# Optimization experiments

Hardware: AMD Instinct MI355X
Metric: run time of the kernel (lower is better)

Reference implementation:

```python
import jax, jax.numpy as jnp
import numpy as np

HEADS, DH = 8, 32

def _ln(x):
    m = x.mean(-1, keepdims=True)
    v = ((x - m) ** 2).mean(-1, keepdims=True)
    return (x - m) * jax.lax.rsqrt(v + 1e-5)

def _attn(xq, xk, ei, ea, wq, wk, wv, we, wo):
    # one relation: q from dst-type nodes xq, k/v from src-type nodes xk
    Nd, Ns, E = xq.shape[0], xk.shape[0], ea.shape[0]
    src, dst = ei[0], ei[1]
    q = (xq @ wq).reshape(Nd, HEADS, DH)
    k = (xk @ wk).reshape(Ns, HEADS, DH)
    v = (xk @ wv).reshape(Ns, HEADS, DH)
    e = (ea @ we).reshape(E, HEADS, DH)
    s = jnp.sum(q[dst] * (k[src] + e), axis=-1) * (DH ** -0.5)  # (E, heads)
    m = jax.ops.segment_max(s, dst, num_segments=Nd)
    m = jnp.where(jnp.isfinite(m), m, 0.0)
    ex = jnp.exp(s - m[dst])
    den = jax.ops.segment_sum(ex, dst, num_segments=Nd)
    msg = jax.ops.segment_sum(ex[:, :, None] * (v[src] + e), dst, num_segments=Nd)
    msg = msg / (den[:, :, None] + 1e-9)
    return msg.reshape(Nd, HEADS * DH) @ wo

def setup_inputs() -> dict:
    key = jax.random.key(0)
    ks = list(jax.random.split(key, 24))
    N, H, ED, L, F = 18432, 256, 64, 2, 512
    EA, ES = 294912, 65536
    nrm = lambda k, shp, s=1.0: jax.random.normal(k, shp, dtype=jnp.float32) * s
    inp = {}
    inp['all_feats_left'] = nrm(ks[0], (N, H))
    inp['all_feats_right'] = nrm(ks[1], (N, H))
    inp['ea_ll'] = nrm(ks[2], (EA, ED))
    inp['ea_rr'] = nrm(ks[3], (EA, ED))
    inp['ea_lr'] = nrm(ks[4], (ES, ED))
    inp['ea_rl'] = nrm(ks[5], (ES, ED))
    inp['ei_ll'] = jax.random.randint(ks[6], (2, EA), 0, N, dtype=jnp.int32)
    inp['ei_rr'] = jax.random.randint(ks[7], (2, EA), 0, N, dtype=jnp.int32)
    inp['ei_lr'] = jax.random.randint(ks[8], (2, ES), 0, N, dtype=jnp.int32)
    inp['ei_rl'] = jax.random.randint(ks[9], (2, ES), 0, N, dtype=jnp.int32)
    # relation order: 0=ll, 1=rr, 2=lr (src left -> dst right), 3=rl
    inp['Wq'] = nrm(ks[10], (L, 4, H, H), H ** -0.5)
    inp['Wk'] = nrm(ks[11], (L, 4, H, H), H ** -0.5)
    inp['Wv'] = nrm(ks[12], (L, 4, H, H), H ** -0.5)
    inp['We'] = nrm(ks[13], (L, 4, ED, H), ED ** -0.5)
    inp['Wo'] = nrm(ks[14], (L, 4, H, H), H ** -0.5)
    inp['ffn_w1'] = nrm(ks[15], (L, 2, H, F), H ** -0.5)
    inp['ffn_b1'] = jnp.zeros((L, 2, F), jnp.float32)
    inp['ffn_w2'] = nrm(ks[16], (L, 2, F, H), F ** -0.5)
    inp['ffn_b2'] = jnp.zeros((L, 2, H), jnp.float32)
    inp['head_w1'] = nrm(ks[17], (H, H), H ** -0.5)
    inp['head_b1'] = jnp.zeros((H,), jnp.float32)
    inp['head_w2'] = nrm(ks[18], (H, 7), H ** -0.5)
    inp['head_b2'] = jnp.zeros((7,), jnp.float32)
    inp['action_start'] = 2048  # slice(K, None), K current nodes per arm
    return inp

def reference(all_feats_left, all_feats_right, ea_ll, ea_rr, ea_lr, ea_rl,
              Wq, Wk, Wv, We, Wo, ffn_w1, ffn_b1, ffn_w2, ffn_b2,
              head_w1, head_b1, head_w2, head_b2,
              ei_ll, ei_rr, ei_lr, ei_rl, action_start):
    xl, xr = all_feats_left, all_feats_right
    L = Wq.shape[0]
    for l in range(L):
        agg_l = (_attn(xl, xl, ei_ll, ea_ll, Wq[l, 0], Wk[l, 0], Wv[l, 0], We[l, 0], Wo[l, 0])
                 + _attn(xl, xr, ei_rl, ea_rl, Wq[l, 3], Wk[l, 3], Wv[l, 3], We[l, 3], Wo[l, 3]))
        agg_r = (_attn(xr, xr, ei_rr, ea_rr, Wq[l, 1], Wk[l, 1], Wv[l, 1], We[l, 1], Wo[l, 1])
                 + _attn(xr, xl, ei_lr, ea_lr, Wq[l, 2], Wk[l, 2], Wv[l, 2], We[l, 2], Wo[l, 2]))
        xl = _ln(xl + agg_l)
        xr = _ln(xr + agg_r)
        xl = _ln(xl + jax.nn.gelu(xl @ ffn_w1[l, 0] + ffn_b1[l, 0]) @ ffn_w2[l, 0] + ffn_b2[l, 0])
        xr = _ln(xr + jax.nn.gelu(xr @ ffn_w1[l, 1] + ffn_b1[l, 1]) @ ffn_w2[l, 1] + ffn_b2[l, 1])
    la = xl[action_start:]
    ra = xr[action_start:]
    head = lambda z: jax.nn.gelu(z @ head_w1 + head_b1) @ head_w2 + head_b2
    return head(la), head(ra)
```

## Files before the change

kernel.cpp:

```cpp
#include <hip/hip_runtime.h>
#include <math.h>

typedef __attribute__((ext_vector_type(8))) short short8;
typedef __attribute__((ext_vector_type(4))) float f32x4;

__device__ __forceinline__ unsigned short f2bf(float f) {
  unsigned u = __builtin_bit_cast(unsigned, f);
  u += 0x7fff + ((u >> 16) & 1);
  return (unsigned short)(u >> 16);
}
__device__ __forceinline__ float bf2f(unsigned short h) {
  unsigned u = ((unsigned)h) << 16;
  return __builtin_bit_cast(float, u);
}
__device__ __forceinline__ float gelu_f(float x) {
  const float c0 = 0.7978845608028654f;
  return 0.5f * x * (1.0f + tanhf(c0 * (x + 0.044715f * x * x * x)));
}
__device__ __forceinline__ void gload16(const unsigned short* g, unsigned short* l) {
  __builtin_amdgcn_global_load_lds(
      (const __attribute__((address_space(1))) unsigned int*)g,
      (__attribute__((address_space(3))) unsigned int*)l, 16, 0, 0);
}

template<bool BIAS, bool GELU>
__global__ __launch_bounds__(256)
void gemm_mfma2_k(const unsigned short* __restrict__ A0, const unsigned short* __restrict__ A1,
                  int lda,
                  const unsigned short* __restrict__ BT0, const unsigned short* __restrict__ BT1,
                  const float* __restrict__ bias0, const float* __restrict__ bias1,
                  float* __restrict__ Cf0, float* __restrict__ Cf1, int Sf, int ldf,
                  unsigned short* __restrict__ Cb10, unsigned short* __restrict__ Cb11,
                  int S2, int ldb1,
                  unsigned short* __restrict__ Cb20, unsigned short* __restrict__ Cb21, int ldb2,
                  int M, int N, int K)
{
  const int z = blockIdx.z;
  const unsigned short* A  = z ? A1  : A0;
  const unsigned short* BT = z ? BT1 : BT0;
  const float* bias        = z ? bias1 : bias0;
  float* Cf                = z ? Cf1 : Cf0;
  unsigned short* Cb1      = z ? Cb11 : Cb10;
  unsigned short* Cb2      = z ? Cb21 : Cb20;

  __shared__ __align__(16) unsigned short As[128 * 32];
  __shared__ __align__(16) unsigned short Bs[128 * 32];
  const int tid = threadIdx.x;
  const int bm = blockIdx.x * 128, bn = blockIdx.y * 128;
  const int lane = tid & 63, w = tid >> 6;
  const int wr = w >> 1, wc = w & 1;
  const int l15 = lane & 15, kg = lane >> 4;

  const int srow0 = w * 16 + (lane >> 2);
  const int srow1 = 64 + srow0;
  const int sslot = lane & 3;
  const int koff0 = (((sslot - (srow0 >> 1)) & 3)) * 8;
  const int koff1 = (((sslot - (srow1 >> 1)) & 3)) * 8;
  const unsigned short* gA0 = A + (size_t)(bm + srow0) * lda + koff0;
  const unsigned short* gA1 = A + (size_t)(bm + srow1) * lda + koff1;
  const unsigned short* gB0 = BT + (size_t)(bn + srow0) * K + koff0;
  const unsigned short* gB1 = BT + (size_t)(bn + srow1) * K + koff1;
  unsigned short* lA0 = As + w * 512;
  unsigned short* lA1 = As + 2048 + w * 512;
  unsigned short* lB0 = Bs + w * 512;
  unsigned short* lB1 = Bs + 2048 + w * 512;

  int roffA[4], roffB[4];
#pragma unroll
  for (int m = 0; m < 4; ++m) {
    int row = wr * 64 + m * 16 + l15;
    roffA[m] = row * 32 + ((kg + (row >> 1)) & 3) * 8;
  }
#pragma unroll
  for (int n = 0; n < 4; ++n) {
    int col = wc * 64 + n * 16 + l15;
    roffB[n] = col * 32 + ((kg + (col >> 1)) & 3) * 8;
  }

  f32x4 acc[4][4] = {};

  for (int k0 = 0; k0 < K; k0 += 32) {
    gload16(gA0 + k0, lA0);
    gload16(gA1 + k0, lA1);
    gload16(gB0 + k0, lB0);
    gload16(gB1 + k0, lB1);
    __syncthreads();
    short8 af[4], bfr[4];
#pragma unroll
    for (int m = 0; m < 4; ++m) af[m] = *(const short8*)(As + roffA[m]);
#pragma unroll
    for (int n = 0; n < 4; ++n) bfr[n] = *(const short8*)(Bs + roffB[n]);
#pragma unroll
    for (int m = 0; m < 4; ++m)
#pragma unroll
      for (int n = 0; n < 4; ++n)
        acc[m][n] = __builtin_amdgcn_mfma_f32_16x16x32_bf16(af[m], bfr[n], acc[m][n], 0, 0, 0);
    __syncthreads();
  }

#pragma unroll
  for (int m = 0; m < 4; ++m) {
#pragma unroll
    for (int n = 0; n < 4; ++n) {
      int col = bn + wc * 64 + n * 16 + l15;
      float bv = BIAS ? bias[col] : 0.f;
      f32x4 v = acc[m][n];
#pragma unroll
      for (int r2 = 0; r2 < 4; ++r2) {
        int row = bm + wr * 64 + m * 16 + kg * 4 + r2;
        float val = v[r2] + bv;
        if (GELU) val = gelu_f(val);
        if (col < Sf) {
          Cf[(size_t)row * ldf + col] = val;
        } else if (col < S2) {
          Cb1[(size_t)row * ldb1 + (col - Sf)] = f2bf(val);
        } else {
          Cb2[(size_t)row * ldb2 + (col - S2)] = f2bf(val);
        }
      }
    }
  }
}

__global__ __launch_bounds__(256)
void gemm_mfma4_k(const unsigned short* __restrict__ Ax0, const unsigned short* __restrict__ Ax1,
                  const unsigned short* __restrict__ Ax2, const unsigned short* __restrict__ Ax3,
                  const unsigned short* __restrict__ Bx0, const unsigned short* __restrict__ Bx1,
                  const unsigned short* __restrict__ Bx2, const unsigned short* __restrict__ Bx3,
                  unsigned short* __restrict__ Cx0, unsigned short* __restrict__ Cx1,
                  unsigned short* __restrict__ Cx2, unsigned short* __restrict__ Cx3,
                  int ldb01, int ldb23, int N01, int N23, int lda, int K, int M)
{
  const int z = blockIdx.z;
  const unsigned short* A; const unsigned short* BT; unsigned short* C;
  int ldb, Nz;
  if (z == 0)      { A = Ax0; BT = Bx0; C = Cx0; ldb = ldb01; Nz = N01; }
  else if (z == 1) { A = Ax1; BT = Bx1; C = Cx1; ldb = ldb01; Nz = N01; }
  else if (z == 2) { A = Ax2; BT = Bx2; C = Cx2; ldb = ldb23; Nz = N23; }
  else             { A = Ax3; BT = Bx3; C = Cx3; ldb = ldb23; Nz = N23; }
  const int bm = blockIdx.x * 128, bn = blockIdx.y * 128;
  if (bn >= Nz) return;

  __shared__ __align__(16) unsigned short As[128 * 32];
  __shared__ __align__(16) unsigned short Bs[128 * 32];
  const int tid = threadIdx.x;
  const int lane = tid & 63, w = tid >> 6;
  const int wr = w >> 1, wc = w & 1;
  const int l15 = lane & 15, kg = lane >> 4;
  const int srow0 = w * 16 + (lane >> 2);
  const int srow1 = 64 + srow0;
  const int sslot = lane & 3;
  const int koff0 = (((sslot - (srow0 >> 1)) & 3)) * 8;
  const int koff1 = (((sslot - (srow1 >> 1)) & 3)) * 8;
  const unsigned short* gA0 = A + (size_t)(bm + srow0) * lda + koff0;
  const unsigned short* gA1 = A + (size_t)(bm + srow1) * lda + koff1;
  const unsigned short* gB0 = BT + (size_t)(bn + srow0) * K + koff0;
  const unsigned short* gB1 = BT + (size_t)(bn + srow1) * K + koff1;
  unsigned short* lA0 = As + w * 512;
  unsigned short* lA1 = As + 2048 + w * 512;
  unsigned short* lB0 = Bs + w * 512;
// ... 27 lines not shown
    for (int m = 0; m < 4; ++m)
#pragma unroll
      for (int n = 0; n < 4; ++n)
        acc[m][n] = __builtin_amdgcn_mfma_f32_16x16x32_bf16(af[m], bfr[n], acc[m][n], 0, 0, 0);
    __syncthreads();
  }
#pragma unroll
  for (int m = 0; m < 4; ++m) {
#pragma unroll
    for (int n = 0; n < 4; ++n) {
      int col = bn + wc * 64 + n * 16 + l15;
      f32x4 v = acc[m][n];
#pragma unroll
      for (int r2 = 0; r2 < 4; ++r2) {
        int row = bm + wr * 64 + m * 16 + kg * 4 + r2;
        C[(size_t)row * ldb + col] = f2bf(v[r2]);
      }
    }
  }
}

template<bool BIAS>
__global__ __launch_bounds__(256)
void gemm_k2(const float* __restrict__ A0, const float* __restrict__ A1,
             const float* __restrict__ B, const float* __restrict__ bias,
             float* __restrict__ C0, float* __restrict__ C1,
             int M, int N, int K)
{
  const float* A = blockIdx.z ? A1 : A0;
  float* C = blockIdx.z ? C1 : C0;
  __shared__ float As[16][132];
// ... 66 lines not shown
    }
  }
}

__global__ void tc_k(const float* __restrict__ in, unsigned short* __restrict__ out,
                     int K, int N, int inStride, int outStride, int rowOff, int totK, int kOff)
{
  const int mat = blockIdx.y;
  const int idx = blockIdx.x * 256 + threadIdx.x;
  if (idx >= N * K) return;
  const int n = idx / K, k = idx - n * K;
  out[(size_t)mat * outStride + (size_t)(rowOff + n) * totK + kOff + k] =
      f2bf(in[(size_t)mat * inStride + (size_t)k * N + n]);
}

__global__ void tc_qkv_k(const float* __restrict__ Wq, const float* __restrict__ Wk,
                         const float* __restrict__ Wv, unsigned short* __restrict__ out)
{
  const int zz = blockIdx.z;
  const float* in = (zz == 0) ? Wq : (zz == 1) ? Wk : Wv;
  const int rowOff = (zz == 0) ? 0 : (zz == 1) ? 768 : 1024;
  const int mat = blockIdx.y;
  const int idx = blockIdx.x * 256 + threadIdx.x;
  const int n = idx >> 8, k = idx & 255;
  out[(size_t)mat * 327680 + (size_t)(rowOff + n) * 256 + k] =
      f2bf(in[(size_t)mat * 65536 + (size_t)k * 256 + n]);
}

__global__ __launch_bounds__(256)
void wqe_k(unsigned short* __restrict__ BT, const float* __restrict__ We, int matStride)
{
  const int mat = blockIdx.y;
  const int oc = blockIdx.x;
  const int g = oc >> 6, cc = oc & 63;
  const int kin = threadIdx.x;
  const float* wrow = We + (size_t)mat * 16384 + (size_t)cc * 256 + g * 32;
  const unsigned short* bq = BT + (size_t)mat * matStride + (size_t)(g * 32) * 256 + kin;
  float acc = 0.f;
#pragma unroll 8
  for (int d = 0; d < 32; ++d)
    acc += bf2f(bq[(size_t)d * 256]) * wrow[d];
  BT[(size_t)mat * matStride + (size_t)(256 + oc) * 256 + kin] = f2bf(acc);
}

__global__ void wo_tc_k(const float* __restrict__ Wo, unsigned short* __restrict__ BTwoF)
{
  const int mat = blockIdx.y;
  const int idx = blockIdx.x * 256 + threadIdx.x;
  const int n = idx >> 8, k = idx & 255;
  const int l = mat >> 2, i = mat & 3;
  const int side = (i == 1 || i == 2) ? 1 : 0;
  const int base = (i >= 2) ? 768 : 0;
  BTwoF[(size_t)(l * 2 + side) * 393216 + (size_t)n * 1536 + base + k] =
      f2bf(Wo[(size_t)mat * 65536 + (size_t)k * 256 + n]);
}

__global__ __launch_bounds__(256)
// ... 4 lines not shown
  const int j = blockIdx.x;
  const int h = j >> 6, c = j & 63;
  const int n = threadIdx.x;
  const float* wep = We + (size_t)mat * 16384 + (size_t)c * 256 + h * 32;
  const float* wop = Wo + (size_t)mat * 65536 + (size_t)(h * 32) * 256 + n;
  float acc = 0.f;
#pragma unroll 8
  for (int d = 0; d < 32; ++d)
    acc += wep[d] * wop[(size_t)d * 256];
  const int l = mat >> 2, i = mat & 3;
  const int side = (i == 1 || i == 2) ? 1 : 0;
  const int base = (i >= 2) ? 768 : 0;
  BTwoF[(size_t)(l * 2 + side) * 393216 + (size_t)n * 1536 + base + 256 + j] = f2bf(acc);
}

template<bool EABF>
__global__ __launch_bounds__(256)
void edge2_k(const int* __restrict__ o0, const int* __restrict__ o1,
             const int2* __restrict__ p0, const int2* __restrict__ p1,
             const void* __restrict__ e0, const void* __restrict__ e1,
             unsigned short* q0, unsigned short* q1,
             const unsigned short* __restrict__ k0, const unsigned short* __restrict__ k1,
             int Nn)
{
  const int y = blockIdx.y;
  const int* offs = y ? o1 : o0;
  const int2* pairs = y ? p1 : p0;
  const void* eaP = y ? e1 : e0;
  unsigned short* qTmsg = y ? q1 : q0;
  const unsigned short* kv = y ? k1 : k0;
  const int wv = (blockIdx.x * blockDim.x + threadIdx.x) >> 6;
  if (wv >= Nn) return;
  const int lane = threadIdx.x & 63;
  const int g = lane >> 3, p = lane & 7;
  const float scale = 0.17677669529663687f;
  const ushort4 qu = *(const ushort4*)(qTmsg + (size_t)wv * 1536 + lane * 4);
  const float qx = bf2f(qu.x), qy = bf2f(qu.y), qz = bf2f(qu.z), qw = bf2f(qu.w);
  const unsigned short* Tp = qTmsg + (size_t)wv * 1536 + 256 + g * 64 + p * 8;
  const ushort4 tu0 = *(const ushort4*)Tp;
  const ushort4 tu1 = *(const ushort4*)(Tp + 4);
  const float Ta0 = bf2f(tu0.x), Ta1 = bf2f(tu0.y), Ta2 = bf2f(tu0.z), Ta3 = bf2f(tu0.w);
  const float Tc0 = bf2f(tu1.x), Tc1 = bf2f(tu1.y), Tc2 = bf2f(tu1.z), Tc3 = bf2f(tu1.w);
  float m = -INFINITY, den = 0.f;
  float ax = 0.f, ay = 0.f, az = 0.f, aw = 0.f;
  float G[8] = {0,0,0,0,0,0,0,0};
  const int e0i = __builtin_amdgcn_readfirstlane(offs[wv]);
  const int e1i = __builtin_amdgcn_readfirstlane(offs[wv + 1]);
  for (int j = e0i; j < e1i; j += 2) {
    const bool hasB = (j + 1) < e1i;
    const int2 prA = pairs[j];
    const int2 prB = hasB ? pairs[j + 1] : prA;
    float eA[8], eB[8];
    if (EABF) {
      const unsigned short* ebp = (const unsigned short*)eaP;
      const short8 eAu = *(const short8*)(ebp + (size_t)prA.x * 64 + p * 8);
      const short8 eBu = *(const short8*)(ebp + (size_t)prB.x * 64 + p * 8);
#pragma unroll
      for (int i = 0; i < 8; ++i) {
        eA[i] = bf2f((unsigned short)eAu[i]);
        eB[i] = bf2f((unsigned short)eBu[i]);
      }
    } else {
      const float* efp = (const float*)eaP;
      const float4 a0 = *(const float4*)(efp + (size_t)prA.x * 64 + p * 8);
      const float4 a1 = *(const float4*)(efp + (size_t)prA.x * 64 + p * 8 + 4);
      const float4 b0 = *(const float4*)(efp + (size_t)prB.x * 64 + p * 8);
      const float4 b1 = *(const float4*)(efp + (size_t)prB.x * 64 + p * 8 + 4);
      eA[0]=a0.x; eA[1]=a0.y; eA[2]=a0.z; eA[3]=a0.w;
      eA[4]=a1.x; eA[5]=a1.y; eA[6]=a1.z; eA[7]=a1.w;
      eB[0]=b0.x; eB[1]=b0.y; eB[2]=b0.z; eB[3]=b0.w;
      eB[4]=b1.x; eB[5]=b1.y; eB[6]=b1.z; eB[7]=b1.w;
    }
    const unsigned short* kpA = kv + (size_t)prA.y * 512 + lane * 4;
    const unsigned short* kpB = kv + (size_t)prB.y * 512 + lane * 4;
    const ushort4 kAu = *(const ushort4*)kpA;
    const ushort4 vAu = *(const ushort4*)(kpA + 256);
    const ushort4 kBu = *(const ushort4*)kpB;
    const ushort4 vBu = *(const ushort4*)(kpB + 256);
    float pA = qx * bf2f(kAu.x) + qy * bf2f(kAu.y) + qz * bf2f(kAu.z) + qw * bf2f(kAu.w);
    pA += eA[0]*Ta0 + eA[1]*Ta1 + eA[2]*Ta2 + eA[3]*Ta3;
    pA += eA[4]*Tc0 + eA[5]*Tc1 + eA[6]*Tc2 + eA[7]*Tc3;
    float pB = qx * bf2f(kBu.x) + qy * bf2f(kBu.y) + qz * bf2f(kBu.z) + qw * bf2f(kBu.w);
    pB += eB[0]*Ta0 + eB[1]*Ta1 + eB[2]*Ta2 + eB[3]*Ta3;
    pB += eB[4]*Tc0 + eB[5]*Tc1 + eB[6]*Tc2 + eB[7]*Tc3;
    pA += __shfl_xor(pA, 1, 64); pA += __shfl_xor(pA, 2, 64); pA += __shfl_xor(pA, 4, 64);
    pB += __shfl_xor(pB, 1, 64); pB += __shfl_xor(pB, 2, 64); pB += __shfl_xor(pB, 4, 64);
    const float sA = pA * scale;
    const float sB = hasB ? pB * scale : -INFINITY;
    const float mn = fmaxf(m, fmaxf(sA, sB));
    const float corr = __expf(m - mn);
    const float wA = __expf(sA - mn);
    const float wB = __expf(sB - mn);
    m = mn;
    den = den * corr + wA + wB;
    ax = ax * corr + wA * bf2f(vAu.x) + wB * bf2f(vBu.x);
    ay = ay * corr + wA * bf2f(vAu.y) + wB * bf2f(vBu.y);
    az = az * corr + wA * bf2f(vAu.z) + wB * bf2f(vBu.z);
    aw = aw * corr + wA * bf2f(vAu.w) + wB * bf2f(vBu.w);
#pragma unroll
    for (int i = 0; i < 8; ++i)
      G[i] = G[i] * corr + wA * eA[i] + wB * eB[i];
  }
  const float inv = 1.f / (den + 1e-9f);
  ushort4 o;
  o.x = f2bf(ax * inv); o.y = f2bf(ay * inv);
  o.z = f2bf(az * inv); o.w = f2bf(aw * inv);
  *(ushort4*)(qTmsg + (size_t)wv * 1536 + lane * 4) = o;
  short8 gn;
#pragma unroll
  for (int i = 0; i < 8; ++i) gn[i] = (short)f2bf(G[i] * inv);
  *(short8*)(qTmsg + (size_t)wv * 1536 + 256 + g * 64 + p * 8) = gn;
}

__global__ __launch_bounds__(256)
void add_ln2_k(unsigned short* __restrict__ xbL, const unsigned short* __restrict__ addL,
               unsigned short* __restrict__ xbR, const unsigned short* __restrict__ addR, int Nn)
// ... 23 lines not shown
  ob.z = f2bf(d.z * r); ob.w = f2bf(d.w * r);
  *(ushort4*)(xb + (size_t)wv * 256 + lane * 4) = ob;
}

__global__ void cvt_x2_k(const float* __restrict__ aL, unsigned short* __restrict__ xbL,
                         const float* __restrict__ aR, unsigned short* __restrict__ xbR, int n4)
{
  const float* a = blockIdx.y ? aR : aL;
  unsigned short* xb = blockIdx.y ? xbR : xbL;
  int i = blockIdx.x * 256 + threadIdx.x;
  if (i >= n4) return;
  float4 v = ((const float4*)a)[i];
  ushort4 b;
  b.x = f2bf(v.x); b.y = f2bf(v.y); b.z = f2bf(v.z); b.w = f2bf(v.w);
  ((ushort4*)xb)[i] = b;
}

__global__ void cvt_ea1_k(const float* __restrict__ src, unsigned short* __restrict__ dst, int n8)
{
  int i = blockIdx.x * 256 + threadIdx.x;
  if (i >= n8) return;
  float4 a = ((const float4*)src)[i * 2];
  float4 b = ((const float4*)src)[i * 2 + 1];
  short8 o;
  o[0] = (short)f2bf(a.x); o[1] = (short)f2bf(a.y);
  o[2] = (short)f2bf(a.z); o[3] = (short)f2bf(a.w);
  o[4] = (short)f2bf(b.x); o[5] = (short)f2bf(b.y);
  o[6] = (short)f2bf(b.z); o[7] = (short)f2bf(b.w);
  *(short8*)(dst + (size_t)i * 8) = o;
}

__global__ void zero4_k(int* p, int n) {
  int i = blockIdx.x * 256 + threadIdx.x;
  if (i < n) p[i] = 0;
}
__global__ void hist4_k(const int* d0, const int* d1, const int* d2, const int* d3,
                        int E0, int E1, int E2, int E3, int* cnt, int Nn) {
  const int s = blockIdx.y;
  const int* d = (s == 0) ? d0 : (s == 1) ? d1 : (s == 2) ? d2 : d3;
  const int E = (s == 0) ? E0 : (s == 1) ? E1 : (s == 2) ? E2 : E3;
  int e = blockIdx.x * 256 + threadIdx.x;
  if (e < E) atomicAdd(&cnt[s * Nn + d[e]], 1);
}
__global__ __launch_bounds__(256)
// ... 72 lines not shown
  const int astart = Nn - Mh;
  float* out = (float*)d_out;

  char* wsp = (char*)d_ws;
  auto alloc = [&](size_t bytes) -> void* {
    void* pp = (void*)wsp;
    wsp += (bytes + 255) & ~(size_t)255;
    return pp;
  };
  unsigned short* xlb = (unsigned short*)alloc((size_t)Nn * 256 * 2);
  unsigned short* xrb = (unsigned short*)alloc((size_t)Nn * 256 * 2);
  unsigned short* aggLb = (unsigned short*)alloc((size_t)Nn * 256 * 2);
  unsigned short* aggRb = (unsigned short*)alloc((size_t)Nn * 256 * 2);
  unsigned short* qTmsgA = (unsigned short*)alloc((size_t)Nn * 1536 * 2);
  unsigned short* qTmsgB = (unsigned short*)alloc((size_t)Nn * 1536 * 2);
  unsigned short* kvbA = (unsigned short*)alloc((size_t)Nn * 512 * 2);
  unsigned short* kvbB = (unsigned short*)alloc((size_t)Nn * 512 * 2);
  unsigned short* BTqkvT = (unsigned short*)alloc((size_t)8 * 1280 * 256 * 2);
  unsigned short* BTwoF  = (unsigned short*)alloc((size_t)4 * 256 * 1536 * 2);
  unsigned short* BTf1   = (unsigned short*)alloc((size_t)4 * 512 * 256 * 2);
  unsigned short* BTf2   = (unsigned short*)alloc((size_t)4 * 256 * 512 * 2);
  unsigned short* BTh1   = (unsigned short*)alloc((size_t)256 * 256 * 2);
  unsigned short* eabf0  = (unsigned short*)alloc((size_t)E[0] * 64 * 2);
  int* offs4 = (int*)alloc((size_t)4 * (Nn + 1) * 4);
  int* cnt4  = (int*)alloc((size_t)4 * Nn * 4);
  int* cur4  = (int*)alloc((size_t)4 * Nn * 4);
  int2* pairs[4];
  for (int s = 0; s < 4; ++s) pairs[s] = (int2*)alloc((size_t)E[s] * 8);

  const dim3 B256(256);
  const int wgNodes = (Nn * 64 + 255) / 256;
  int maxE = E[0];
  for (int s = 1; s < 4; ++s) if (E[s] > maxE) maxE = E[s];

  cvt_x2_k<<<dim3((Nn * 64 + 255) / 256, 2), B256, 0, stream>>>(afl, xlb, afr, xrb, Nn * 64);
  cvt_ea1_k<<<dim3((E[0] * 8 + 255) / 256), B256, 0, stream>>>(eaA[0], eabf0, E[0] * 8);
  zero4_k<<<dim3((4 * Nn + 255) / 256), B256, 0, stream>>>(cnt4, 4 * Nn);
  {
    dim3 gh((maxE + 255) / 256, 4);
    hist4_k<<<gh, B256, 0, stream>>>(eiA[0] + E[0], eiA[1] + E[1], eiA[2] + E[2], eiA[3] + E[3],
                                     E[0], E[1], E[2], E[3], cnt4, Nn);
    scan4_k<<<dim3(4), B256, 0, stream>>>(cnt4, offs4, cur4, Nn);
    scatter4_k<<<gh, B256, 0, stream>>>(eiA[0], eiA[1], eiA[2], eiA[3],
                                        E[0], E[1], E[2], E[3], cur4,
                                        pairs[0], pairs[1], pairs[2], pairs[3], Nn);
  }
  {
    tc_qkv_k<<<dim3(256, 8, 3), B256, 0, stream>>>(Wq, Wk, Wv, BTqkvT);
    wqe_k<<<dim3(512, 8), B256, 0, stream>>>(BTqkvT, We, 327680);
    wo_tc_k<<<dim3(256, 8), B256, 0, stream>>>(Wo, BTwoF);
    wc_k<<<dim3(512, 8), B256, 0, stream>>>(We, Wo, BTwoF);
    tc_k<<<dim3((131072 + 255) / 256, 4), B256, 0, stream>>>(fw1, BTf1, 256, 512, 131072, 131072, 0, 256, 0);
    tc_k<<<dim3((131072 + 255) / 256, 4), B256, 0, stream>>>(fw2, BTf2, 512, 256, 131072, 131072, 0, 512, 0);
    tc_k<<<dim3((65536 + 255) / 256, 1), B256, 0, stream>>>(hw1, BTh1, 256, 256, 0, 0, 0, 256, 0);
  }

  auto mfma2 = [&](const unsigned short* A0, const unsigned short* A1, int lda,
                   const unsigned short* BT0, const unsigned short* BT1,
                   const float* bias0, const float* bias1,
                   float* Cf0, float* Cf1, int Sf, int ldf,
                   unsigned short* Cb10, unsigned short* Cb11, int S2, int ldb1,
                   unsigned short* Cb20, unsigned short* Cb21, int ldb2,
                   int M, int N, int K, bool biasf, bool gelu) {
    dim3 g(M / 128, N / 128, 2);
    if (biasf && gelu)
      gemm_mfma2_k<true, true ><<<g, B256, 0, stream>>>(A0, A1, lda, BT0, BT1, bias0, bias1,
          Cf0, Cf1, Sf, ldf, Cb10, Cb11, S2, ldb1, Cb20, Cb21, ldb2, M, N, K);
    else if (biasf)
      gemm_mfma2_k<true, false><<<g, B256, 0, stream>>>(A0, A1, lda, BT0, BT1, bias0, bias1,
          Cf0, Cf1, Sf, ldf, Cb10, Cb11, S2, ldb1, Cb20, Cb21, ldb2, M, N, K);
    else
      gemm_mfma2_k<false, false><<<g, B256, 0, stream>>>(A0, A1, lda, BT0, BT1, bias0, bias1,
          Cf0, Cf1, Sf, ldf, Cb10, Cb11, S2, ldb1, Cb20, Cb21, ldb2, M, N, K);
  };

  for (int l = 0; l < 2; ++l) {
    const unsigned short* btLL = BTqkvT + (size_t)(l*4+0) * 327680;
    const unsigned short* btRR = BTqkvT + (size_t)(l*4+1) * 327680;
    const unsigned short* btLR = BTqkvT + (size_t)(l*4+2) * 327680;
    const unsigned short* btRL = BTqkvT + (size_t)(l*4+3) * 327680;
    mfma2(xlb, xrb, 256, btLL, btRR, nullptr, nullptr, nullptr, nullptr, 0, 0,
          qTmsgA, qTmsgB, 768, 1536, kvbA, kvbB, 512, Nn, 1280, 256, false, false);
    edge2_k<true><<<dim3(wgNodes, 1), B256, 0, stream>>>(
        offs4, offs4, pairs[0], pairs[0], eabf0, eabf0, qTmsgA, qTmsgA, kvbA, kvbA, Nn);
    edge2_k<false><<<dim3(wgNodes, 1), B256, 0, stream>>>(
        offs4 + (size_t)(Nn + 1), offs4 + (size_t)(Nn + 1), pairs[1], pairs[1],
        eaA[1], eaA[1], qTmsgB, qTmsgB, kvbB, kvbB, Nn);
    gemm_mfma4_k<<<dim3(Nn / 128, 6, 4), B256, 0, stream>>>(
        xlb, xrb, xrb, xlb,
        btRL, btLR, btRL + (size_t)768 * 256, btLR + (size_t)768 * 256,
        qTmsgA + 768, qTmsgB + 768, kvbA, kvbB,
        1536, 512, 768, 512, 256, 256, Nn);
    edge2_k<false><<<dim3(wgNodes, 2), B256, 0, stream>>>(
        offs4 + (size_t)3 * (Nn + 1), offs4 + (size_t)2 * (Nn + 1), pairs[3], pairs[2],
        eaA[3], eaA[2], qTmsgA + 768, qTmsgB + 768, kvbA, kvbB, Nn);
    mfma2(qTmsgA, qTmsgB, 1536, BTwoF + (size_t)(l*2+0)*393216, BTwoF + (size_t)(l*2+1)*393216,
          nullptr, nullptr, nullptr, nullptr, 0, 0, aggLb, aggRb, 256, 256,
          nullptr, nullptr, 0, Nn, 256, 1536, false, false);
    add_ln2_k<<<dim3(wgNodes, 2), B256, 0, stream>>>(xlb, aggLb, xrb, aggRb, Nn);
    const int fL = l * 2 + 0, fR = l * 2 + 1;
    mfma2(xlb, xrb, 256, BTf1 + (size_t)fL*131072, BTf1 + (size_t)fR*131072,
          fb1 + (size_t)fL*512, fb1 + (size_t)fR*512, nullptr, nullptr, 0, 0,
          nullptr, nullptr, 0, 0, kvbA, kvbB, 512, Nn, 512, 256, true, true);
    mfma2(kvbA, kvbB, 512, BTf2 + (size_t)fL*131072, BTf2 + (size_t)fR*131072,
          fb2 + (size_t)fL*256, fb2 + (size_t)fR*256, nullptr, nullptr, 0, 0,
          aggLb, aggRb, 256, 256, nullptr, nullptr, 0, Nn, 256, 512, true, false);
    add_ln2_k<<<dim3(wgNodes, 2), B256, 0, stream>>>(xlb, aggLb, xrb, aggRb, Nn);
  }
  float* h1L = (float*)kvbA;
  float* h1R = (float*)kvbB;
  mfma2(xlb + (size_t)astart * 256, xrb + (size_t)astart * 256, 256, BTh1, BTh1,
        hb1, hb1, h1L, h1R, 256, 256, nullptr, nullptr, 0, 0, nullptr, nullptr, 0,
        Mh, 256, 256, true, true);
  gemm_k2<true><<<dim3(Mh / 128, 1, 2), B256, 0, stream>>>(h1L, h1R, hw2, hb2,
                                                           out, out + (size_t)Mh * 7, Mh, 7, 256);
}
```

Measured before the change: 1.162 ms.

## Fuse all per-layer QKV projections into one GEMM and four edge relations into one launch

Packs the self and cross relation Q/K/V weights for each side into one 2560-column transposed matrix and computes them in a single GEMM launch. The K and V outputs are written interleaved so the edge kernel can fetch both with one 16-byte load. All four relation edge-attention passes now run in one launch with separate K/V buffers per relation. The bf16 conversion of edge attributes for relation 0 is dropped, so every relation reads fp32 edge features. This trades extra edge-feature bandwidth for fewer launches, more parallelism per launch and better load vectorisation.

```diff
diff --git a/kernel.cpp b/kernel.cpp
--- a/kernel.cpp
+++ b/kernel.cpp
@@ -22,128 +22,32 @@
       (const __attribute__((address_space(1))) unsigned int*)g,
       (__attribute__((address_space(3))) unsigned int*)l, 16, 0, 0);
 }
-
-template<bool BIAS, bool GELU>
+__device__ __forceinline__ int ileave512(int cc) {
+  const int base = (cc & 256) ? 4 : 0;
+  const int c2 = cc & 255;
+  return (c2 >> 2) * 8 + base + (c2 & 3);
+}
+
 __global__ __launch_bounds__(256)
-void gemm_mfma2_k(const unsigned short* __restrict__ A0, const unsigned short* __restrict__ A1,
-                  int lda,
-                  const unsigned short* __restrict__ BT0, const unsigned short* __restrict__ BT1,
-                  const float* __restrict__ bias0, const float* __restrict__ bias1,
-                  float* __restrict__ Cf0, float* __restrict__ Cf1, int Sf, int ldf,
-                  unsigned short* __restrict__ Cb10, unsigned short* __restrict__ Cb11,
-                  int S2, int ldb1,
-                  unsigned short* __restrict__ Cb20, unsigned short* __restrict__ Cb21, int ldb2,
-                  int M, int N, int K)
+void gemm_qkv_k(const unsigned short* __restrict__ A0, const unsigned short* __restrict__ A1,
+                const unsigned short* __restrict__ BT0, const unsigned short* __restrict__ BT1,
+                unsigned short* __restrict__ qT0, unsigned short* __restrict__ qT1,
+                unsigned short* __restrict__ kvS0, unsigned short* __restrict__ kvS1,
+                unsigned short* __restrict__ kvX0, unsigned short* __restrict__ kvX1,
+                int M)
 {
   const int z = blockIdx.z;
   const unsigned short* A  = z ? A1  : A0;
   const unsigned short* BT = z ? BT1 : BT0;
-  const float* bias        = z ? bias1 : bias0;
-  float* Cf                = z ? Cf1 : Cf0;
-  unsigned short* Cb1      = z ? Cb11 : Cb10;
-  unsigned short* Cb2      = z ? Cb21 : Cb20;
+  unsigned short* qT  = z ? qT1  : qT0;
+  unsigned short* kvS = z ? kvS1 : kvS0;
+  unsigned short* kvX = z ? kvX1 : kvX0;
+  const int K = 256, lda = 256;
 
   __shared__ __align__(16) unsigned short As[128 * 32];
   __shared__ __align__(16) unsigned short Bs[128 * 32];
   const int tid = threadIdx.x;
   const int bm = blockIdx.x * 128, bn = blockIdx.y * 128;
-  const int lane = tid & 63, w = tid >> 6;
-  const int wr = w >> 1, wc = w & 1;
-  const int l15 = lane & 15, kg = lane >> 4;
-
-  const int srow0 = w * 16 + (lane >> 2);
-  const int srow1 = 64 + srow0;
-  const int sslot = lane & 3;
-  const int koff0 = (((sslot - (srow0 >> 1)) & 3)) * 8;
-  const int koff1 = (((sslot - (srow1 >> 1)) & 3)) * 8;
-  const unsigned short* gA0 = A + (size_t)(bm + srow0) * lda + koff0;
-  const unsigned short* gA1 = A + (size_t)(bm + srow1) * lda + koff1;
-  const unsigned short* gB0 = BT + (size_t)(bn + srow0) * K + koff0;
-  const unsigned short* gB1 = BT + (size_t)(bn + srow1) * K + koff1;
-  unsigned short* lA0 = As + w * 512;
-  unsigned short* lA1 = As + 2048 + w * 512;
-  unsigned short* lB0 = Bs + w * 512;
-  unsigned short* lB1 = Bs + 2048 + w * 512;
-
-  int roffA[4], roffB[4];
-#pragma unroll
-  for (int m = 0; m < 4; ++m) {
-    int row = wr * 64 + m * 16 + l15;
-    roffA[m] = row * 32 + ((kg + (row >> 1)) & 3) * 8;
-  }
-#pragma unroll
-  for (int n = 0; n < 4; ++n) {
-    int col = wc * 64 + n * 16 + l15;
-    roffB[n] = col * 32 + ((kg + (col >> 1)) & 3) * 8;
-  }
-
-  f32x4 acc[4][4] = {};
-
-  for (int k0 = 0; k0 < K; k0 += 32) {
-    gload16(gA0 + k0, lA0);
-    gload16(gA1 + k0, lA1);
-    gload16(gB0 + k0, lB0);
-    gload16(gB1 + k0, lB1);
-    __syncthreads();
-    short8 af[4], bfr[4];
-#pragma unroll
-    for (int m = 0; m < 4; ++m) af[m] = *(const short8*)(As + roffA[m]);
-#pragma unroll
-    for (int n = 0; n < 4; ++n) bfr[n] = *(const short8*)(Bs + roffB[n]);
-#pragma unroll
-    for (int m = 0; m < 4; ++m)
-#pragma unroll
-      for (int n = 0; n < 4; ++n)
-        acc[m][n] = __builtin_amdgcn_mfma_f32_16x16x32_bf16(af[m], bfr[n], acc[m][n], 0, 0, 0);
-    __syncthreads();
-  }
-
-#pragma unroll
-  for (int m = 0; m < 4; ++m) {
-#pragma unroll
-    for (int n = 0; n < 4; ++n) {
-      int col = bn + wc * 64 + n * 16 + l15;
-      float bv = BIAS ? bias[col] : 0.f;
-      f32x4 v = acc[m][n];
-#pragma unroll
-      for (int r2 = 0; r2 < 4; ++r2) {
-        int row = bm + wr * 64 + m * 16 + kg * 4 + r2;
-        float val = v[r2] + bv;
-        if (GELU) val = gelu_f(val);
-        if (col < Sf) {
-          Cf[(size_t)row * ldf + col] = val;
-        } else if (col < S2) {
-          Cb1[(size_t)row * ldb1 + (col - Sf)] = f2bf(val);
-        } else {
-          Cb2[(size_t)row * ldb2 + (col - S2)] = f2bf(val);
-        }
-      }
-    }
-  }
-}
-
-__global__ __launch_bounds__(256)
-void gemm_mfma4_k(const unsigned short* __restrict__ Ax0, const unsigned short* __restrict__ Ax1,
-                  const unsigned short* __restrict__ Ax2, const unsigned short* __restrict__ Ax3,
-                  const unsigned short* __restrict__ Bx0, const unsigned short* __restrict__ Bx1,
-                  const unsigned short* __restrict__ Bx2, const unsigned short* __restrict__ Bx3,
-                  unsigned short* __restrict__ Cx0, unsigned short* __restrict__ Cx1,
-                  unsigned short* __restrict__ Cx2, unsigned short* __restrict__ Cx3,
-                  int ldb01, int ldb23, int N01, int N23, int lda, int K, int M)
-{
-  const int z = blockIdx.z;
-  const unsigned short* A; const unsigned short* BT; unsigned short* C;
-  int ldb, Nz;
-  if (z == 0)      { A = Ax0; BT = Bx0; C = Cx0; ldb = ldb01; Nz = N01; }
-  else if (z == 1) { A = Ax1; BT = Bx1; C = Cx1; ldb = ldb01; Nz = N01; }
-  else if (z == 2) { A = Ax2; BT = Bx2; C = Cx2; ldb = ldb23; Nz = N23; }
-  else             { A = Ax3; BT = Bx3; C = Cx3; ldb = ldb23; Nz = N23; }
-  const int bm = blockIdx.x * 128, bn = blockIdx.y * 128;
-  if (bn >= Nz) return;
-
-  __shared__ __align__(16) unsigned short As[128 * 32];
-  __shared__ __align__(16) unsigned short Bs[128 * 32];
-  const int tid = threadIdx.x;
   const int lane = tid & 63, w = tid >> 6;
   const int wr = w >> 1, wc = w & 1;
   const int l15 = lane & 15, kg = lane >> 4;
@@ -201,7 +105,112 @@
 #pragma unroll
       for (int r2 = 0; r2 < 4; ++r2) {
         int row = bm + wr * 64 + m * 16 + kg * 4 + r2;
-        C[(size_t)row * ldb + col] = f2bf(v[r2]);
+        unsigned short bv = f2bf(v[r2]);
+        if (col < 768) {
+          qT[(size_t)row * 1536 + col] = bv;
+        } else if (col < 1280) {
+          kvS[(size_t)row * 512 + ileave512(col - 768)] = bv;
+        } else if (col < 2048) {
+          qT[(size_t)row * 1536 + 768 + (col - 1280)] = bv;
+        } else {
+          kvX[(size_t)row * 512 + ileave512(col - 2048)] = bv;
+        }
+      }
+    }
+  }
+}
+
+template<bool BIAS, bool GELU>
+__global__ __launch_bounds__(256)
+void gemm_mfma2_k(const unsigned short* __restrict__ A0, const unsigned short* __restrict__ A1,
+                  int lda,
+                  const unsigned short* __restrict__ BT0, const unsigned short* __restrict__ BT1,
+                  const float* __restrict__ bias0, const float* __restrict__ bias1,
+                  float* __restrict__ Cf0, float* __restrict__ Cf1, int Sf, int ldf,
+                  unsigned short* __restrict__ Cb10, unsigned short* __restrict__ Cb11,
+                  int S2, int ldb1,
+                  unsigned short* __restrict__ Cb20, unsigned short* __restrict__ Cb21, int ldb2,
+                  int M, int N, int K)
+{
+  const int z = blockIdx.z;
+  const unsigned short* A  = z ? A1  : A0;
+  const unsigned short* BT = z ? BT1 : BT0;
+  const float* bias        = z ? bias1 : bias0;
+  float* Cf                = z ? Cf1 : Cf0;
+  unsigned short* Cb1      = z ? Cb11 : Cb10;
+  unsigned short* Cb2      = z ? Cb21 : Cb20;
+
+  __shared__ __align__(16) unsigned short As[128 * 32];
+  __shared__ __align__(16) unsigned short Bs[128 * 32];
+  const int tid = threadIdx.x;
+  const int bm = blockIdx.x * 128, bn = blockIdx.y * 128;
+  const int lane = tid & 63, w = tid >> 6;
+  const int wr = w >> 1, wc = w & 1;
+  const int l15 = lane & 15, kg = lane >> 4;
+  const int srow0 = w * 16 + (lane >> 2);
+  const int srow1 = 64 + srow0;
+  const int sslot = lane & 3;
+  const int koff0 = (((sslot - (srow0 >> 1)) & 3)) * 8;
+  const int koff1 = (((sslot - (srow1 >> 1)) & 3)) * 8;
+  const unsigned short* gA0 = A + (size_t)(bm + srow0) * lda + koff0;
+  const unsigned short* gA1 = A + (size_t)(bm + srow1) * lda + koff1;
+  const unsigned short* gB0 = BT + (size_t)(bn + srow0) * K + koff0;
+  const unsigned short* gB1 = BT + (size_t)(bn + srow1) * K + koff1;
+  unsigned short* lA0 = As + w * 512;
+  unsigned short* lA1 = As + 2048 + w * 512;
+  unsigned short* lB0 = Bs + w * 512;
+  unsigned short* lB1 = Bs + 2048 + w * 512;
+
+  int roffA[4], roffB[4];
+#pragma unroll
+  for (int m = 0; m < 4; ++m) {
+    int row = wr * 64 + m * 16 + l15;
+    roffA[m] = row * 32 + ((kg + (row >> 1)) & 3) * 8;
+  }
+#pragma unroll
+  for (int n = 0; n < 4; ++n) {
+    int col = wc * 64 + n * 16 + l15;
+    roffB[n] = col * 32 + ((kg + (col >> 1)) & 3) * 8;
+  }
+
+  f32x4 acc[4][4] = {};
+  for (int k0 = 0; k0 < K; k0 += 32) {
+    gload16(gA0 + k0, lA0);
+    gload16(gA1 + k0, lA1);
+    gload16(gB0 + k0, lB0);
+    gload16(gB1 + k0, lB1);
+    __syncthreads();
+    short8 af[4], bfr[4];
+#pragma unroll
+    for (int m = 0; m < 4; ++m) af[m] = *(const short8*)(As + roffA[m]);
+#pragma unroll
+    for (int n = 0; n < 4; ++n) bfr[n] = *(const short8*)(Bs + roffB[n]);
+#pragma unroll
+    for (int m = 0; m < 4; ++m)
+#pragma unroll
+      for (int n = 0; n < 4; ++n)
+        acc[m][n] = __builtin_amdgcn_mfma_f32_16x16x32_bf16(af[m], bfr[n], acc[m][n], 0, 0, 0);
+    __syncthreads();
+  }
+#pragma unroll
+  for (int m = 0; m < 4; ++m) {
+#pragma unroll
+    for (int n = 0; n < 4; ++n) {
+      int col = bn + wc * 64 + n * 16 + l15;
+      float bv = BIAS ? bias[col] : 0.f;
+      f32x4 v = acc[m][n];
+#pragma unroll
+      for (int r2 = 0; r2 < 4; ++r2) {
+        int row = bm + wr * 64 + m * 16 + kg * 4 + r2;
+        float val = v[r2] + bv;
+        if (GELU) val = gelu_f(val);
+        if (col < Sf) {
+          Cf[(size_t)row * ldf + col] = val;
+        } else if (col < S2) {
+          Cb1[(size_t)row * ldb1 + (col - Sf)] = f2bf(val);
+        } else {
+          Cb2[(size_t)row * ldb2 + (col - S2)] = f2bf(val);
+        }
       }
     }
   }
@@ -298,33 +307,49 @@
       f2bf(in[(size_t)mat * inStride + (size_t)k * N + n]);
 }
 
-__global__ void tc_qkv_k(const float* __restrict__ Wq, const float* __restrict__ Wk,
-                         const float* __restrict__ Wv, unsigned short* __restrict__ out)
-{
-  const int zz = blockIdx.z;
-  const float* in = (zz == 0) ? Wq : (zz == 1) ? Wk : Wv;
-  const int rowOff = (zz == 0) ? 0 : (zz == 1) ? 768 : 1024;
-  const int mat = blockIdx.y;
+__global__ void tc_all_k(const float* __restrict__ Wq, const float* __restrict__ Wk,
+                         const float* __restrict__ Wv, unsigned short* __restrict__ BTall)
+{
+  const int part = blockIdx.z;
+  const int slot = blockIdx.y;
+  const int l = slot >> 1, zz = slot & 1;
+  const int self = l * 4 + zz;
+  const int crossq = l * 4 + (zz ? 2 : 3);
+  const int crosskv = l * 4 + (zz ? 3 : 2);
+  const float* in; int mat, rowOff;
+  switch (part) {
+    case 0: in = Wq; mat = self;    rowOff = 0;    break;
+    case 1: in = Wk; mat = self;    rowOff = 768;  break;
+    case 2: in = Wv; mat = self;    rowOff = 1024; break;
+    case 3: in = Wq; mat = crossq;  rowOff = 1280; break;
+    case 4: in = Wk; mat = crosskv; rowOff = 2048; break;
+    default:in = Wv; mat = crosskv; rowOff = 2304; break;
+  }
   const int idx = blockIdx.x * 256 + threadIdx.x;
   const int n = idx >> 8, k = idx & 255;
-  out[(size_t)mat * 327680 + (size_t)(rowOff + n) * 256 + k] =
+  BTall[(size_t)slot * 655360 + (size_t)(rowOff + n) * 256 + k] =
       f2bf(in[(size_t)mat * 65536 + (size_t)k * 256 + n]);
 }
 
 __global__ __launch_bounds__(256)
-void wqe_k(unsigned short* __restrict__ BT, const float* __restrict__ We, int matStride)
-{
-  const int mat = blockIdx.y;
+void wqe2_k(unsigned short* __restrict__ BTall, const float* __restrict__ We)
+{
+  const int which = blockIdx.z;
+  const int slot = blockIdx.y;
+  const int l = slot >> 1, zz = slot & 1;
+  const int mat = which ? (l * 4 + (zz ? 2 : 3)) : (l * 4 + zz);
+  const int baseQ = which ? 1280 : 0;
+  const int baseT = which ? 1536 : 256;
   const int oc = blockIdx.x;
   const int g = oc >> 6, cc = oc & 63;
   const int kin = threadIdx.x;
   const float* wrow = We + (size_t)mat * 16384 + (size_t)cc * 256 + g * 32;
-  const unsigned short* bq = BT + (size_t)mat * matStride + (size_t)(g * 32) * 256 + kin;
+  const unsigned short* bq = BTall + (size_t)slot * 655360 + (size_t)(baseQ + g * 32) * 256 + kin;
   float acc = 0.f;
 #pragma unroll 8
   for (int d = 0; d < 32; ++d)
     acc += bf2f(bq[(size_t)d * 256]) * wrow[d];
-  BT[(size_t)mat * matStride + (size_t)(256 + oc) * 256 + kin] = f2bf(acc);
+  BTall[(size_t)slot * 655360 + (size_t)(baseT + oc) * 256 + kin] = f2bf(acc);
 }
 
 __global__ void wo_tc_k(const float* __restrict__ Wo, unsigned short* __restrict__ BTwoF)
@@ -359,21 +384,25 @@
   BTwoF[(size_t)(l * 2 + side) * 393216 + (size_t)n * 1536 + base + 256 + j] = f2bf(acc);
 }
 
-template<bool EABF>
 __global__ __launch_bounds__(256)
-void edge2_k(const int* __restrict__ o0, const int* __restrict__ o1,
+void edge4_k(const int* __restrict__ o0, const int* __restrict__ o1,
+             const int* __restrict__ o2, const int* __restrict__ o3,
              const int2* __restrict__ p0, const int2* __restrict__ p1,
-             const void* __restrict__ e0, const void* __restrict__ e1,
+             const int2* __restrict__ p2, const int2* __restrict__ p3,
+             const float* __restrict__ e0, const float* __restrict__ e1,
+             const float* __restrict__ e2, const float* __restrict__ e3,
              unsigned short* q0, unsigned short* q1,
+             unsigned short* q2, unsigned short* q3,
              const unsigned short* __restrict__ k0, const unsigned short* __restrict__ k1,
+             const unsigned short* __restrict__ k2, const unsigned short* __restrict__ k3,
              int Nn)
 {
   const int y = blockIdx.y;
-  const int* offs = y ? o1 : o0;
-  const int2* pairs = y ? p1 : p0;
-  const void* eaP = y ? e1 : e0;
-  unsigned short* qTmsg = y ? q1 : q0;
-  const unsigned short* kv = y ? k1 : k0;
+  const int* offs = (y == 0) ? o0 : (y == 1) ? o1 : (y == 2) ? o2 : o3;
+  const int2* pairs = (y == 0) ? p0 : (y == 1) ? p1 : (y == 2) ? p2 : p3;
+  const float* ea = (y == 0) ? e0 : (y == 1) ? e1 : (y == 2) ? e2 : e3;
+  unsigned short* qTmsg = (y == 0) ? q0 : (y == 1) ? q1 : (y == 2) ? q2 : q3;
+  const unsigned short* kv = (y == 0) ? k0 : (y == 1) ? k1 : (y == 2) ? k2 : k3;
   const int wv = (blockIdx.x * blockDim.x + threadIdx.x) >> 6;
   if (wv >= Nn) return;
   const int lane = threadIdx.x & 63;
@@ -395,39 +424,22 @@
     const bool hasB = (j + 1) < e1i;
     const int2 prA = pairs[j];
     const int2 prB = hasB ? pairs[j + 1] : prA;
-    float eA[8], eB[8];
-    if (EABF) {
-      const unsigned short* ebp = (const unsigned short*)eaP;
-      const short8 eAu = *(const short8*)(ebp + (size_t)prA.x * 64 + p * 8);
-      const short8 eBu = *(const short8*)(ebp + (size_t)prB.x * 64 + p * 8);
-#pragma unroll
-      for (int i = 0; i < 8; ++i) {
-        eA[i] = bf2f((unsigned short)eAu[i]);
-        eB[i] = bf2f((unsigned short)eBu[i]);
-      }
-    } else {
-      const float* efp = (const float*)eaP;
-      const float4 a0 = *(const float4*)(efp + (size_t)prA.x * 64 + p * 8);
-      const float4 a1 = *(const float4*)(efp + (size_t)prA.x * 64 + p * 8 + 4);
-      const float4 b0 = *(const float4*)(efp + (size_t)prB.x * 64 + p * 8);
-      const float4 b1 = *(const float4*)(efp + (size_t)prB.x * 64 + p * 8 + 4);
-      eA[0]=a0.x; eA[1]=a0.y; eA[2]=a0.z; eA[3]=a0.w;
-      eA[4]=a1.x; eA[5]=a1.y; eA[6]=a1.z; eA[7]=a1.w;
-      eB[0]=b0.x; eB[1]=b0.y; eB[2]=b0.z; eB[3]=b0.w;
-      eB[4]=b1.x; eB[5]=b1.y; eB[6]=b1.z; eB[7]=b1.w;
-    }
-    const unsigned short* kpA = kv + (size_t)prA.y * 512 + lane * 4;
-    const unsigned short* kpB = kv + (size_t)prB.y * 512 + lane * 4;
-    const ushort4 kAu = *(const ushort4*)kpA;
-    const ushort4 vAu = *(const ushort4*)(kpA + 256);
-    const ushort4 kBu = *(const ushort4*)kpB;
-    const ushort4 vBu = *(const ushort4*)(kpB + 256);
-    float pA = qx * bf2f(kAu.x) + qy * bf2f(kAu.y) + qz * bf2f(kAu.z) + qw * bf2f(kAu.w);
-    pA += eA[0]*Ta0 + eA[1]*Ta1 + eA[2]*Ta2 + eA[3]*Ta3;
-    pA += eA[4]*Tc0 + eA[5]*Tc1 + eA[6]*Tc2 + eA[7]*Tc3;
-    float pB = qx * bf2f(kBu.x) + qy * bf2f(kBu.y) + qz * bf2f(kBu.z) + qw * bf2f(kBu.w);
-    pB += eB[0]*Ta0 + eB[1]*Ta1 + eB[2]*Ta2 + eB[3]*Ta3;
-    pB += eB[4]*Tc0 + eB[5]*Tc1 + eB[6]*Tc2 + eB[7]*Tc3;
+    const float* epA = ea + (size_t)prA.x * 64 + p * 8;
+    const float* epB = ea + (size_t)prB.x * 64 + p * 8;
+    const float4 a0 = *(const float4*)epA;
+    const float4 a1 = *(const float4*)(epA + 4);
+    const float4 b0 = *(const float4*)epB;
+    const float4 b1 = *(const float4*)(epB + 4);
+    const short8 kvA = *(const short8*)(kv + (size_t)prA.y * 512 + lane * 8);
+    const short8 kvB = *(const short8*)(kv + (size_t)prB.y * 512 + lane * 8);
+    float pA = qx * bf2f((unsigned short)kvA[0]) + qy * bf2f((unsigned short)kvA[1])
+             + qz * bf2f((unsigned short)kvA[2]) + qw * bf2f((unsigned short)kvA[3]);
+    pA += a0.x*Ta0 + a0.y*Ta1 + a0.z*Ta2 + a0.w*Ta3;
+    pA += a1.x*Tc0 + a1.y*Tc1 + a1.z*Tc2 + a1.w*Tc3;
+    float pB = qx * bf2f((unsigned short)kvB[0]) + qy * bf2f((unsigned short)kvB[1])
+             + qz * bf2f((unsigned short)kvB[2]) + qw * bf2f((unsigned short)kvB[3]);
+    pB += b0.x*Ta0 + b0.y*Ta1 + b0.z*Ta2 + b0.w*Ta3;
+    pB += b1.x*Tc0 + b1.y*Tc1 + b1.z*Tc2 + b1.w*Tc3;
     pA += __shfl_xor(pA, 1, 64); pA += __shfl_xor(pA, 2, 64); pA += __shfl_xor(pA, 4, 64);
     pB += __shfl_xor(pB, 1, 64); pB += __shfl_xor(pB, 2, 64); pB += __shfl_xor(pB, 4, 64);
     const float sA = pA * scale;
@@ -438,13 +450,18 @@
     const float wB = __expf(sB - mn);
     m = mn;
     den = den * corr + wA + wB;
-    ax = ax * corr + wA * bf2f(vAu.x) + wB * bf2f(vBu.x);
-    ay = ay * corr + wA * bf2f(vAu.y) + wB * bf2f(vBu.y);
-    az = az * corr + wA * bf2f(vAu.z) + wB * bf2f(vBu.z);
-    aw = aw * corr + wA * bf2f(vAu.w) + wB * bf2f(vBu.w);
-#pragma unroll
-    for (int i = 0; i < 8; ++i)
-      G[i] = G[i] * corr + wA * eA[i] + wB * eB[i];
+    ax = ax * corr + wA * bf2f((unsigned short)kvA[4]) + wB * bf2f((unsigned short)kvB[4]);
+    ay = ay * corr + wA * bf2f((unsigned short)kvA[5]) + wB * bf2f((unsigned short)kvB[5]);
+    az = az * corr + wA * bf2f((unsigned short)kvA[6]) + wB * bf2f((unsigned short)kvB[6]);
+    aw = aw * corr + wA * bf2f((unsigned short)kvA[7]) + wB * bf2f((unsigned short)kvB[7]);
+    G[0] = G[0] * corr + wA * a0.x + wB * b0.x;
+    G[1] = G[1] * corr + wA * a0.y + wB * b0.y;
+    G[2] = G[2] * corr + wA * a0.z + wB * b0.z;
+    G[3] = G[3] * corr + wA * a0.w + wB * b0.w;
+    G[4] = G[4] * corr + wA * a1.x + wB * b1.x;
+    G[5] = G[5] * corr + wA * a1.y + wB * b1.y;
+    G[6] = G[6] * corr + wA * a1.z + wB * b1.z;
+    G[7] = G[7] * corr + wA * a1.w + wB * b1.w;
   }
   const float inv = 1.f / (den + 1e-9f);
   ushort4 o;
@@ -498,20 +515,6 @@
   ushort4 b;
   b.x = f2bf(v.x); b.y = f2bf(v.y); b.z = f2bf(v.z); b.w = f2bf(v.w);
   ((ushort4*)xb)[i] = b;
-}
-
-__global__ void cvt_ea1_k(const float* __restrict__ src, unsigned short* __restrict__ dst, int n8)
-{
-  int i = blockIdx.x * 256 + threadIdx.x;
-  if (i >= n8) return;
-  float4 a = ((const float4*)src)[i * 2];
-  float4 b = ((const float4*)src)[i * 2 + 1];
-  short8 o;
-  o[0] = (short)f2bf(a.x); o[1] = (short)f2bf(a.y);
-  o[2] = (short)f2bf(a.z); o[3] = (short)f2bf(a.w);
-  o[4] = (short)f2bf(b.x); o[5] = (short)f2bf(b.y);
-  o[6] = (short)f2bf(b.z); o[7] = (short)f2bf(b.w);
-  *(short8*)(dst + (size_t)i * 8) = o;
 }
 
 __global__ void zero4_k(int* p, int n) {
@@ -614,14 +617,15 @@
   unsigned short* aggRb = (unsigned short*)alloc((size_t)Nn * 256 * 2);
   unsigned short* qTmsgA = (unsigned short*)alloc((size_t)Nn * 1536 * 2);
   unsigned short* qTmsgB = (unsigned short*)alloc((size_t)Nn * 1536 * 2);
-  unsigned short* kvbA = (unsigned short*)alloc((size_t)Nn * 512 * 2);
-  unsigned short* kvbB = (unsigned short*)alloc((size_t)Nn * 512 * 2);
-  unsigned short* BTqkvT = (unsigned short*)alloc((size_t)8 * 1280 * 256 * 2);
-  unsigned short* BTwoF  = (unsigned short*)alloc((size_t)4 * 256 * 1536 * 2);
-  unsigned short* BTf1   = (unsigned short*)alloc((size_t)4 * 512 * 256 * 2);
-  unsigned short* BTf2   = (unsigned short*)alloc((size_t)4 * 256 * 512 * 2);
-  unsigned short* BTh1   = (unsigned short*)alloc((size_t)256 * 256 * 2);
-  unsigned short* eabf0  = (unsigned short*)alloc((size_t)E[0] * 64 * 2);
+  unsigned short* kvSA = (unsigned short*)alloc((size_t)Nn * 512 * 2);
+  unsigned short* kvSB = (unsigned short*)alloc((size_t)Nn * 512 * 2);
+  unsigned short* kvXL = (unsigned short*)alloc((size_t)Nn * 512 * 2);
+  unsigned short* kvXR = (unsigned short*)alloc((size_t)Nn * 512 * 2);
+  unsigned short* BTall = (unsigned short*)alloc((size_t)4 * 655360 * 2);
+  unsigned short* BTwoF = (unsigned short*)alloc((size_t)4 * 256 * 1536 * 2);
+  unsigned short* BTf1  = (unsigned short*)alloc((size_t)4 * 512 * 256 * 2);
+  unsigned short* BTf2  = (unsigned short*)alloc((size_t)4 * 256 * 512 * 2);
+  unsigned short* BTh1  = (unsigned short*)alloc((size_t)256 * 256 * 2);
   int* offs4 = (int*)alloc((size_t)4 * (Nn + 1) * 4);
   int* cnt4  = (int*)alloc((size_t)4 * Nn * 4);
   int* cur4  = (int*)alloc((size_t)4 * Nn * 4);
@@ -634,7 +638,6 @@
   for (int s = 1; s < 4; ++s) if (E[s] > maxE) maxE = E[s];
 
   cvt_x2_k<<<dim3((Nn * 64 + 255) / 256, 2), B256, 0, stream>>>(afl, xlb, afr, xrb, Nn * 64);
-  cvt_ea1_k<<<dim3((E[0] * 8 + 255) / 256), B256, 0, stream>>>(eaA[0], eabf0, E[0] * 8);
   zero4_k<<<dim3((4 * Nn + 255) / 256), B256, 0, stream>>>(cnt4, 4 * Nn);
   {
     dim3 gh((maxE + 255) / 256, 4);
@@ -646,8 +649,8 @@
                                         pairs[0], pairs[1], pairs[2], pairs[3], Nn);
   }
   {
-    tc_qkv_k<<<dim3(256, 8, 3), B256, 0, stream>>>(Wq, Wk, Wv, BTqkvT);
-    wqe_k<<<dim3(512, 8), B256, 0, stream>>>(BTqkvT, We, 327680);
+    tc_all_k<<<dim3(256, 4, 6), B256, 0, stream>>>(Wq, Wk, Wv, BTall);
+    wqe2_k<<<dim3(512, 4, 2), B256, 0, stream>>>(BTall, We);
     wo_tc_k<<<dim3(256, 8), B256, 0, stream>>>(Wo, BTwoF);
     wc_k<<<dim3(512, 8), B256, 0, stream>>>(We, Wo, BTwoF);
     tc_k<<<dim3((131072 + 255) / 256, 4), B256, 0, stream>>>(fw1, BTf1, 256, 512, 131072, 131072, 0, 256, 0);
@@ -675,25 +678,16 @@
   };
 
   for (int l = 0; l < 2; ++l) {
-    const unsigned short* btLL = BTqkvT + (size_t)(l*4+0) * 327680;
-    const unsigned short* btRR = BTqkvT + (size_t)(l*4+1) * 327680;
-    const unsigned short* btLR = BTqkvT + (size_t)(l*4+2) * 327680;
-    const unsigned short* btRL = BTqkvT + (size_t)(l*4+3) * 327680;
-    mfma2(xlb, xrb, 256, btLL, btRR, nullptr, nullptr, nullptr, nullptr, 0, 0,
-          qTmsgA, qTmsgB, 768, 1536, kvbA, kvbB, 512, Nn, 1280, 256, false, false);
-    edge2_k<true><<<dim3(wgNodes, 1), B256, 0, stream>>>(
-        offs4, offs4, pairs[0], pairs[0], eabf0, eabf0, qTmsgA, qTmsgA, kvbA, kvbA, Nn);
-    edge2_k<false><<<dim3(wgNodes, 1), B256, 0, stream>>>(
-        offs4 + (size_t)(Nn + 1), offs4 + (size_t)(Nn + 1), pairs[1], pairs[1],
-        eaA[1], eaA[1], qTmsgB, qTmsgB, kvbB, kvbB, Nn);
-    gemm_mfma4_k<<<dim3(Nn / 128, 6, 4), B256, 0, stream>>>(
-        xlb, xrb, xrb, xlb,
-        btRL, btLR, btRL + (size_t)768 * 256, btLR + (size_t)768 * 256,
-        qTmsgA + 768, qTmsgB + 768, kvbA, kvbB,
-        1536, 512, 768, 512, 256, 256, Nn);
-    edge2_k<false><<<dim3(wgNodes, 2), B256, 0, stream>>>(
-        offs4 + (size_t)3 * (Nn + 1), offs4 + (size_t)2 * (Nn + 1), pairs[3], pairs[2],
-        eaA[3], eaA[2], qTmsgA + 768, qTmsgB + 768, kvbA, kvbB, Nn);
+    gemm_qkv_k<<<dim3(Nn / 128, 20, 2), B256, 0, stream>>>(
+        xlb, xrb,
+        BTall + (size_t)(l * 2 + 0) * 655360, BTall + (size_t)(l * 2 + 1) * 655360,
+        qTmsgA, qTmsgB, kvSA, kvSB, kvXL, kvXR, Nn);
+    edge4_k<<<dim3(wgNodes, 4), B256, 0, stream>>>(
+        offs4, offs4 + (size_t)(Nn + 1), offs4 + (size_t)3 * (Nn + 1), offs4 + (size_t)2 * (Nn + 1),
+        pairs[0], pairs[1], pairs[3], pairs[2],
+        eaA[0], eaA[1], eaA[3], eaA[2],
+        qTmsgA, qTmsgB, qTmsgA + 768, qTmsgB + 768,
+        kvSA, kvSB, kvXR, kvXL, Nn);
     mfma2(qTmsgA, qTmsgB, 1536, BTwoF + (size_t)(l*2+0)*393216, BTwoF + (size_t)(l*2+1)*393216,
           nullptr, nullptr, nullptr, nullptr, 0, 0, aggLb, aggRb, 256, 256,
           nullptr, nullptr, 0, Nn, 256, 1536, false, false);
@@ -701,14 +695,14 @@
     const int fL = l * 2 + 0, fR = l * 2 + 1;
     mfma2(xlb, xrb, 256, BTf1 + (size_t)fL*131072, BTf1 + (size_t)fR*131072,
           fb1 + (size_t)fL*512, fb1 + (size_t)fR*512, nullptr, nullptr, 0, 0,
-          nullptr, nullptr, 0, 0, kvbA, kvbB, 512, Nn, 512, 256, true, true);
-    mfma2(kvbA, kvbB, 512, BTf2 + (size_t)fL*131072, BTf2 + (size_t)fR*131072,
+          kvSA, kvSB, 512, 512, nullptr, nullptr, 0, Nn, 512, 256, true, true);
+    mfma2(kvSA, kvSB, 512, BTf2 + (size_t)fL*131072, BTf2 + (size_t)fR*131072,
           fb2 + (size_t)fL*256, fb2 + (size_t)fR*256, nullptr, nullptr, 0, 0,
           aggLb, aggRb, 256, 256, nullptr, nullptr, 0, Nn, 256, 512, true, false);
     add_ln2_k<<<dim3(wgNodes, 2), B256, 0, stream>>>(xlb, aggLb, xrb, aggRb, Nn);
   }
-  float* h1L = (float*)kvbA;
-  float* h1R = (float*)kvbB;
+  float* h1L = (float*)kvSA;
+  float* h1R = (float*)kvSB;
   mfma2(xlb + (size_t)astart * 256, xrb + (size_t)astart * 256, 256, BTh1, BTh1,
         hb1, hb1, h1L, h1R, 256, 256, nullptr, nullptr, 0, 0, nullptr, nullptr, 0,
         Mh, 256, 256, true, true);
```

After: 1.106 ms. 1.05x faster.
